# Kernel tuning notes

Measured on AMD Instinct MI355X. Metric: run time of the kernel, lower is better.

The kernel has to match this reference:

```python
import jax, jax.numpy as jnp
import numpy as np

B, S, V, D, H, C, NH = 8, 512, 32000, 768, 768, 9, 8
DH = D // NH


def setup_inputs() -> dict:
    key = jax.random.key(0)
    ks = list(jax.random.split(key, 24))
    it = iter(ks)

    def w(shape, s=0.02):
        return jax.random.normal(next(it), shape, jnp.float32) * s

    return {
        "input_ids": jax.random.randint(next(it), (B, S), 0, V, dtype=jnp.int32),
        "labels": jax.random.randint(next(it), (B, S), 0, C, dtype=jnp.int32),
        "emb_table": w((V, D), 1.0),
        "hw_Wh": w((D, D)),
        "hw_bh": jnp.zeros((D,), jnp.float32),
        "hw_Wt": w((D, D)),
        "hw_bt": jnp.zeros((D,), jnp.float32),
        "in_proj_w": w((3 * D, D)),
        "in_proj_b": jnp.zeros((3 * D,), jnp.float32),
        "out_proj_w": w((D, D)),
        "out_proj_b": jnp.zeros((D,), jnp.float32),
        "lstm0_Wih": w((2, 4 * H, D)),
        "lstm0_Whh": w((2, 4 * H, H)),
        "lstm0_b": jnp.zeros((2, 4 * H), jnp.float32),
        "lstm1_Wih": w((2, 4 * H, 2 * H)),
        "lstm1_Whh": w((2, 4 * H, H)),
        "lstm1_b": jnp.zeros((2, 4 * H), jnp.float32),
        "fc_W": w((C, 2 * H)),
        "fc_b": jnp.zeros((C,), jnp.float32),
        "crf_start": w((C,), 0.1),
        "crf_end": w((C,), 0.1),
        "crf_trans": w((C, C), 0.1),
    }


def _lstm_dir(x, Wih, Whh, b, reverse):
    # x: [B,S,in] -> outputs [B,S,H]; PyTorch gate order i,f,g,o
    xt = x.transpose(1, 0, 2)  # [S,B,in]
    h0 = jnp.zeros((x.shape[0], H), x.dtype)

    def step(carry, xt_):
        h, c = carry
        g = xt_ @ Wih.T + h @ Whh.T + b
        i, f, gg, o = jnp.split(g, 4, axis=-1)
        c = jax.nn.sigmoid(f) * c + jax.nn.sigmoid(i) * jnp.tanh(gg)
        h = jax.nn.sigmoid(o) * jnp.tanh(c)
        return (h, c), h

    _, hs = jax.lax.scan(step, (h0, h0), xt, reverse=reverse)
    return hs.transpose(1, 0, 2)


def _bilstm_layer(x, Wih, Whh, b):
    fwd = _lstm_dir(x, Wih[0], Whh[0], b[0], False)
    bwd = _lstm_dir(x, Wih[1], Whh[1], b[1], True)
    return jnp.concatenate([fwd, bwd], axis=-1)


def _emissions(input_ids, emb_table, hw_Wh, hw_bh, hw_Wt, hw_bt,
               in_proj_w, in_proj_b, out_proj_w, out_proj_b,
               lstm0_Wih, lstm0_Whh, lstm0_b, lstm1_Wih, lstm1_Whh, lstm1_b,
               fc_W, fc_b):
    x = emb_table[input_ids]  # [B,S,D]
    # Highway (1 layer, relu)
    hh = jax.nn.relu(x @ hw_Wh.T + hw_bh)
    t = jax.nn.sigmoid(x @ hw_Wt.T + hw_bt)
    x = t * hh + (1.0 - t) * x
    # Multi-head self-attention
    qkv = x @ in_proj_w.T + in_proj_b
    q, k, v = jnp.split(qkv, 3, axis=-1)
    hd = lambda a: a.reshape(B, S, NH, DH).transpose(0, 2, 1, 3)  # [B,NH,S,DH]
    q, k, v = hd(q), hd(k), hd(v)
    att = jax.nn.softmax(jnp.einsum('bhqd,bhkd->bhqk', q, k) / np.float32(np.sqrt(DH)), axis=-1)
    o = jnp.einsum('bhqk,bhkd->bhqd', att, v).transpose(0, 2, 1, 3).reshape(B, S, D)
    x = o @ out_proj_w.T + out_proj_b
    # 2-layer BiLSTM (inference: dropout off)
    x = _bilstm_layer(x, lstm0_Wih, lstm0_Whh, lstm0_b)
    x = _bilstm_layer(x, lstm1_Wih, lstm1_Whh, lstm1_b)
    return x @ fc_W.T + fc_b  # [B,S,C]


def _crf_nll(emissions, tags, crf_start, crf_end, crf_trans):
    # full mask (labels==-100 replaced by 0 before mask built), reduction='sum'
    em_t = emissions.transpose(1, 0, 2)  # [S,B,C]
    num = crf_start[tags[:, 0]] + crf_end[tags[:, -1]]
    num = num + jnp.take_along_axis(emissions, tags[..., None], axis=-1)[..., 0].sum(-1)
    num = num + crf_trans[tags[:, :-1], tags[:, 1:]].sum(-1)
    a0 = crf_start + em_t[0]  # [B,C]

    def fstep(a, em):
        a = jax.scipy.special.logsumexp(a[:, :, None] + crf_trans[None], axis=1) + em
        return a, None

    aT, _ = jax.lax.scan(fstep, a0, em_t[1:])
    logZ = jax.scipy.special.logsumexp(aT + crf_end, axis=-1)
    return -(num - logZ).sum()


def _viterbi(emissions, crf_start, crf_end, crf_trans):
    em_t = emissions.transpose(1, 0, 2)  # [S,B,C]
    s0 = crf_start + em_t[0]

    def vstep(s, em):
        sc = s[:, :, None] + crf_trans[None]  # [B,C_prev,C_next]
        return jnp.max(sc, axis=1) + em, jnp.argmax(sc, axis=1)

    sT, bps = jax.lax.scan(vstep, s0, em_t[1:])  # bps: [S-1,B,C]
    last = jnp.argmax(sT + crf_end, axis=-1)  # [B]

    def bstep(tag, bp):
        prev = jnp.take_along_axis(bp, tag[:, None], axis=1)[:, 0]
        return prev, prev

    _, path = jax.lax.scan(bstep, last, bps, reverse=True)  # [S-1,B]
    return jnp.concatenate([path, last[None]], axis=0).transpose(1, 0)  # [B,S]


def reference(input_ids, labels, emb_table, hw_Wh, hw_bh, hw_Wt, hw_bt,
              in_proj_w, in_proj_b, out_proj_w, out_proj_b,
              lstm0_Wih, lstm0_Whh, lstm0_b, lstm1_Wih, lstm1_Whh, lstm1_b,
              fc_W, fc_b, crf_start, crf_end, crf_trans):
    emissions = _emissions(input_ids, emb_table, hw_Wh, hw_bh, hw_Wt, hw_bt,
                           in_proj_w, in_proj_b, out_proj_w, out_proj_b,
                           lstm0_Wih, lstm0_Whh, lstm0_b,
                           lstm1_Wih, lstm1_Whh, lstm1_b, fc_W, fc_b)
    loss = _crf_nll(emissions, labels, crf_start, crf_end, crf_trans)
    decode = _viterbi(emissions, crf_start, crf_end, crf_trans)
    return loss, decode
```

## Files before the change

### kernel.cpp

```cpp
#include <hip/hip_runtime.h>
#include <hip/hip_bf16.h>
#include <cstdint>

#define B_   8
#define S_   512
#define D_   768
#define C_   9
#define BS_  4096

typedef unsigned long long u64;
typedef unsigned short ushort_t;
typedef short bf16x8 __attribute__((ext_vector_type(8)));
typedef float f32x4 __attribute__((ext_vector_type(4)));
typedef __attribute__((address_space(1))) const void gvoid_t;
typedef __attribute__((address_space(3))) void svoid_t;

__global__ __launch_bounds__(192) void k_embed(const int* __restrict__ ids,
                                               const float* __restrict__ emb,
                                               float* __restrict__ x) {
  int row = blockIdx.x;
  int id = ids[row];
  const float4* src = (const float4*)(emb + (size_t)id * D_);
  float4* dst = (float4*)(x + (size_t)row * D_);
  dst[threadIdx.x] = src[threadIdx.x];
}

#define GIDX(k, m) ((k)*144 + (m) + (((m) >> 5) << 2))

__global__ __launch_bounds__(256) void k_gemm(const float* __restrict__ A,
                                              const float* __restrict__ W,
                                              const float* __restrict__ bias,
                                              float* __restrict__ C,
                                              int M, int N, int K, int act, int mode) {
  __shared__ float As[2304];
  __shared__ float Bs[2304];
  int nwg = gridDim.x * gridDim.y;
  int lin = blockIdx.y * gridDim.x + blockIdx.x;
  int cpx = nwg >> 3;
  int swz = (lin & 7) * cpx + (lin >> 3);
  int bxs = swz % gridDim.x, bys = swz / gridDim.x;
  int bm0 = bys * 128, bn0 = bxs * 128;
  int tid = threadIdx.x;
  int tm = tid >> 4, tn = tid & 15;
  float acc[8][8];
#pragma unroll
  for (int i = 0; i < 8; ++i)
#pragma unroll
    for (int j = 0; j < 8; ++j) acc[i][j] = 0.f;

  for (int k0 = 0; k0 < K; k0 += 16) {
    __syncthreads();
#pragma unroll
    for (int j = 0; j < 2; ++j) {
      int f4 = tid + j * 256;
      int r = f4 >> 2;
      int kq = (f4 & 3) * 4;
      float4 va = *(const float4*)(A + (size_t)(bm0 + r) * K + k0 + kq);
      As[GIDX(kq + 0, r)] = va.x; As[GIDX(kq + 1, r)] = va.y;
      As[GIDX(kq + 2, r)] = va.z; As[GIDX(kq + 3, r)] = va.w;
      float4 vb = *(const float4*)(W + (size_t)(bn0 + r) * K + k0 + kq);
      Bs[GIDX(kq + 0, r)] = vb.x; Bs[GIDX(kq + 1, r)] = vb.y;
      Bs[GIDX(kq + 2, r)] = vb.z; Bs[GIDX(kq + 3, r)] = vb.w;
    }
    __syncthreads();
#pragma unroll
    for (int kk = 0; kk < 16; ++kk) {
      float a[8], b[8];
      *(float4*)&a[0] = *(const float4*)&As[GIDX(kk, tm * 8)];
      *(float4*)&a[4] = *(const float4*)&As[GIDX(kk, tm * 8 + 4)];
      *(float4*)&b[0] = *(const float4*)&Bs[GIDX(kk, tn * 8)];
      *(float4*)&b[4] = *(const float4*)&Bs[GIDX(kk, tn * 8 + 4)];
#pragma unroll
      for (int i = 0; i < 8; ++i)
#pragma unroll
        for (int j = 0; j < 8; ++j) acc[i][j] += a[i] * b[j];
    }
  }

  float bv[8];
#pragma unroll
  for (int j = 0; j < 8; ++j) bv[j] = bias[bn0 + tn * 8 + j];
#pragma unroll
  for (int i = 0; i < 8; ++i) {
    int row = bm0 + tm * 8 + i;
    float o[8];
#pragma unroll
    for (int j = 0; j < 8; ++j) {
      float v = acc[i][j] + bv[j];
      if (act == 1) v = fmaxf(v, 0.f);
      else if (act == 2) v = 1.f / (1.f + expf(-v));
      o[j] = v;
    }
    if (mode == 0) {
      float* cp = C + (size_t)row * N + bn0 + tn * 8;
      *(float4*)cp = make_float4(o[0], o[1], o[2], o[3]);
      *(float4*)(cp + 4) = make_float4(o[4], o[5], o[6], o[7]);
    } else {
      int bb = row >> 9, t = row & 511;
#pragma unroll
      for (int j = 0; j < 8; ++j) {
        unsigned n = bn0 + tn * 8 + j;
        unsigned dir = n / 3072u;
        unsigned n2 = n - dir * 3072u;
        unsigned g = n2 / 768u;
        unsigned rem = n2 - g * 768u;
        unsigned grp = rem >> 3, u = rem & 7;
        C[(((size_t)(dir * 512 + t) * 96 + grp) << 8) + u * 32 + g * 8 + bb] = o[j];
      }
    }
  }
}

__device__ inline ushort_t f2bf_bits(float x) {
  __hip_bfloat16 h = __float2bfloat16(x);
  return __builtin_bit_cast(ushort_t, h);
}
__device__ inline float bf2f(ushort_t b) {
  return __bfloat162float(__builtin_bit_cast(__hip_bfloat16, b));
}

__global__ __launch_bounds__(256) void k_cvt(const float* __restrict__ src,
                                             ushort_t* __restrict__ dst,
                                             int K, int total4, int mode) {
  int kq4 = K >> 2;
  for (int idx = blockIdx.x * 256 + threadIdx.x; idx < total4; idx += gridDim.x * 256) {
    int m = idx / kq4;
    int kq = (idx - m * kq4) * 4;
    float4 v = *(const float4*)(src + (size_t)m * K + kq);
    ushort4 hi, lo;
    hi.x = f2bf_bits(v.x); lo.x = f2bf_bits(v.x - bf2f(hi.x));
    hi.y = f2bf_bits(v.y); lo.y = f2bf_bits(v.y - bf2f(hi.y));
    hi.z = f2bf_bits(v.z); lo.z = f2bf_bits(v.z - bf2f(hi.z));
    hi.w = f2bf_bits(v.w); lo.w = f2bf_bits(v.w - bf2f(hi.w));
    ushort_t* base = dst + (size_t)m * 3 * K + kq;
    *(ushort4*)(base)         = hi;
    *(ushort4*)(base + K)     = mode ? hi : lo;
    *(ushort4*)(base + 2 * K) = mode ? lo : hi;
  }
}

__global__ __launch_bounds__(256) void k_mfma(const ushort_t* __restrict__ A,
                                              const ushort_t* __restrict__ W,
                                              const float* __restrict__ bias,
                                              float* __restrict__ C,
                                              int N, int Kp, int act, int mode) {
  __shared__ ushort_t Asb[128 * 64];
  __shared__ ushort_t Bsb[128 * 64];
  int nwg = gridDim.x * gridDim.y;
  int lin = blockIdx.y * gridDim.x + blockIdx.x;
  int cpx = nwg >> 3;
  int swz = (lin & 7) * cpx + (lin >> 3);
  int bn0 = (swz % gridDim.x) * 128, bm0 = (swz / gridDim.x) * 128;
  int tid = threadIdx.x;
  int w = tid >> 6, lane = tid & 63;
  int lr = lane & 15, lq = lane >> 4;

  f32x4 acc[2][8];
#pragma unroll
  for (int i = 0; i < 2; ++i)
#pragma unroll
    for (int j = 0; j < 8; ++j) acc[i][j] = (f32x4){0.f, 0.f, 0.f, 0.f};

  int srow0 = tid >> 3;
  int sc = tid & 7;

  for (int k0 = 0; k0 < Kp; k0 += 64) {
    __syncthreads();
#pragma unroll
    for (int it = 0; it < 4; ++it) {
      int row = it * 32 + srow0;
      int soff = (sc ^ (row & 7)) * 8;
      const ushort_t* ga = A + (size_t)(bm0 + row) * Kp + k0 + soff;
      const ushort_t* gb = W + (size_t)(bn0 + row) * Kp + k0 + soff;
      char* la = (char*)Asb + it * 4096 + (tid & 192) * 16;
      char* lb = (char*)Bsb + it * 4096 + (tid & 192) * 16;
      __builtin_amdgcn_global_load_lds((gvoid_t*)ga, (svoid_t*)la, 16, 0, 0);
      __builtin_amdgcn_global_load_lds((gvoid_t*)gb, (svoid_t*)lb, 16, 0, 0);
    }
    __syncthreads();
#pragma unroll
    for (int kf = 0; kf < 2; ++kf) {
      int c = kf * 4 + lq;
      int rowA0 = w * 32 + lr;
      int rowA1 = rowA0 + 16;
      bf16x8 a0 = *(const bf16x8*)&Asb[rowA0 * 64 + ((c ^ (rowA0 & 7)) << 3)];
      bf16x8 a1 = *(const bf16x8*)&Asb[rowA1 * 64 + ((c ^ (rowA1 & 7)) << 3)];
#pragma unroll
      for (int ns = 0; ns < 8; ++ns) {
        int rowB = ns * 16 + lr;
        bf16x8 b = *(const bf16x8*)&Bsb[rowB * 64 + ((c ^ (rowB & 7)) << 3)];
        acc[0][ns] = __builtin_amdgcn_mfma_f32_16x16x32_bf16(a0, b, acc[0][ns], 0, 0, 0);
        acc[1][ns] = __builtin_amdgcn_mfma_f32_16x16x32_bf16(a1, b, acc[1][ns], 0, 0, 0);
      }
    }
  }

  if (mode == 1) {
#pragma unroll
    for (int ns = 0; ns < 8; ++ns) {
      unsigned n = bn0 + ns * 16 + lr;
      unsigned dir = n / 3072u;
      unsigned n2 = n - dir * 3072u;
      unsigned g = n2 / 768u;
      unsigned rem = n2 - g * 768u;
      unsigned grp = rem >> 3, u = rem & 7;
      float bv = bias[n];
#pragma unroll
      for (int ms = 0; ms < 2; ++ms) {
#pragma unroll
        for (int r = 0; r < 4; ++r) {
          int m = bm0 + w * 32 + ms * 16 + lq * 4 + r;
          int bb = m >> 9, t = m & 511;
          C[(((size_t)(dir * 512 + t) * 96 + grp) << 8) + u * 32 + g * 8 + bb] =
              acc[ms][ns][r] + bv;
        }
      }
    }
  } else {
#pragma unroll
    for (int ns = 0; ns < 8; ++ns) {
      int col = bn0 + ns * 16 + lr;
      float bv = bias[col];
#pragma unroll
      for (int ms = 0; ms < 2; ++ms) {
#pragma unroll
        for (int r = 0; r < 4; ++r) {
          int m = bm0 + w * 32 + ms * 16 + lq * 4 + r;
          float v = acc[ms][ns][r] + bv;
          if (act == 1) v = fmaxf(v, 0.f);
          else if (act == 2) v = 1.f / (1.f + expf(-v));
          C[(size_t)m * N + col] = v;
        }
      }
    }
  }
}

__global__ __launch_bounds__(256) void k_highway(float* __restrict__ x,
                                                 const float* __restrict__ hh,
                                                 const float* __restrict__ tt) {
  const int n4 = BS_ * D_ / 4;
  for (int i = blockIdx.x * 256 + threadIdx.x; i < n4; i += gridDim.x * 256) {
    float4 xv = ((const float4*)x)[i];
    float4 hv = ((const float4*)hh)[i];
    float4 tv = ((const float4*)tt)[i];
    xv.x = tv.x * hv.x + (1.f - tv.x) * xv.x;
    xv.y = tv.y * hv.y + (1.f - tv.y) * xv.y;
    xv.z = tv.z * hv.z + (1.f - tv.z) * xv.z;
    xv.w = tv.w * hv.w + (1.f - tv.w) * xv.w;
    ((float4*)x)[i] = xv;
  }
}

__global__ __launch_bounds__(256) void k_attn(const float* __restrict__ qkv,
                                              float* __restrict__ out) {
  __shared__ float Qs[16 * 100];
  __shared__ float Ks[32 * 101];
  __shared__ float Ps[16 * 513];
  int bh = blockIdx.x;
  int b = bh >> 3, h = bh & 7;
  int q0 = blockIdx.y * 16;
  int tid = threadIdx.x;
  const float scale = 0.10206207261596577f;

  const float* qb = qkv + (size_t)(b * 512 + q0) * 2304 + h * 96;
  for (int i = tid; i < 16 * 96; i += 256) {
    int r = i / 96, c = i - r * 96;
    Qs[r * 100 + c] = qb[(size_t)r * 2304 + c];
  }
  int qi = tid >> 4, kseg = tid & 15;

  for (int kt = 0; kt < 16; ++kt) {
    __syncthreads();
    const float* kb = qkv + (size_t)(b * 512 + kt * 32) * 2304 + 768 + h * 96;
    for (int i = tid; i < 32 * 96; i += 256) {
      int r = i / 96, c = i - r * 96;
      Ks[r * 101 + c] = kb[(size_t)r * 2304 + c];
    }
    __syncthreads();
    int kj0 = kseg * 2;
    float s0 = 0.f, s1 = 0.f;
    const float* qrow = &Qs[qi * 100];
    const float* k0p = &Ks[kj0 * 101];
    const float* k1p = &Ks[(kj0 + 1) * 101];
#pragma unroll 8
    for (int d = 0; d < 96; ++d) {
      float qv = qrow[d];
      s0 += qv * k0p[d];
      s1 += qv * k1p[d];
    }
    Ps[qi * 513 + kt * 32 + kj0] = s0 * scale;
    Ps[qi * 513 + kt * 32 + kj0 + 1] = s1 * scale;
  }
  __syncthreads();

  {
    float m = -1e30f;
    for (int j = 0; j < 32; ++j) m = fmaxf(m, Ps[qi * 513 + kseg + j * 16]);
    m = fmaxf(m, __shfl_xor(m, 1)); m = fmaxf(m, __shfl_xor(m, 2));
    m = fmaxf(m, __shfl_xor(m, 4)); m = fmaxf(m, __shfl_xor(m, 8));
    float sum = 0.f;
    for (int j = 0; j < 32; ++j) {
      int idx = qi * 513 + kseg + j * 16;
      float e = expf(Ps[idx] - m);
      Ps[idx] = e;
      sum += e;
    }
    sum += __shfl_xor(sum, 1); sum += __shfl_xor(sum, 2);
    sum += __shfl_xor(sum, 4); sum += __shfl_xor(sum, 8);
    float inv = 1.f / sum;
    for (int j = 0; j < 32; ++j) Ps[qi * 513 + kseg + j * 16] *= inv;
  }

  float acc[6] = {0.f, 0.f, 0.f, 0.f, 0.f, 0.f};
  int d0 = kseg * 6;
  for (int kt = 0; kt < 16; ++kt) {
    __syncthreads();
    const float* vb = qkv + (size_t)(b * 512 + kt * 32) * 2304 + 1536 + h * 96;
    for (int i = tid; i < 32 * 96; i += 256) {
      int r = i / 96, c = i - r * 96;
      Ks[r * 101 + c] = vb[(size_t)r * 2304 + c];
    }
    __syncthreads();
#pragma unroll 4
    for (int kj = 0; kj < 32; ++kj) {
      float p = Ps[qi * 513 + kt * 32 + kj];
      const float* vrow = &Ks[kj * 101 + d0];
#pragma unroll
      for (int u = 0; u < 6; ++u) acc[u] += p * vrow[u];
    }
  }
  float* ob = out + (size_t)(b * 512 + q0 + qi) * 768 + h * 96 + d0;
#pragma unroll
  for (int u = 0; u < 6; ++u) ob[u] = acc[u];
}

#define NWGD 96
__global__ __launch_bounds__(256, 1) void k_lstm(const float* __restrict__ gates,
                                                 const float* __restrict__ Whh,
                                                 float* __restrict__ hbuf,
                                                 float* __restrict__ hs,
                                                 int* __restrict__ flags) {
  __shared__ float hlds[8 * 772];
  int tid = threadIdx.x;
  int wg = blockIdx.x;
  int dir = wg / NWGD;
  int grp = wg % NWGD;
  int rg = tid >> 5;
  int ks = tid & 31;

  float4 w4[4][6];
#pragma unroll
  for (int j = 0; j < 4; ++j) {
    const float* wp = Whh + ((size_t)dir * 3072 + j * 768 + grp * 8 + rg) * 768 + ks * 4;
#pragma unroll
    for (int jj = 0; jj < 6; ++jj)
      w4[j][jj] = *(const float4*)(wp + jj * 128);
  }

  float* hb = hbuf + (size_t)dir * 2 * 6144;
  const float* gbase = gates + (size_t)dir * 512 * 24576 + grp * 256 + tid;
  const float* hp = hlds + ks * 4;
  float cst = 0.f;

  for (int step = 0; step < 512; ++step) {
    int t = dir ? (511 - step) : step;
    float gqv = gbase[(size_t)t * 24576];

#pragma unroll
    for (int i = 0; i < 3; ++i) {
      int idx = i * 256 + tid;
      int b2 = idx / 96;
      int kq = (idx - b2 * 96) * 8;
      const u64* src = (const u64*)(hb + (step & 1) * 6144 + b2 * 768 + kq);
      u64 lo  = __hip_atomic_load(src + 0, __ATOMIC_RELAXED, __HIP_MEMORY_SCOPE_AGENT);
      u64 hi  = __hip_atomic_load(src + 1, __ATOMIC_RELAXED, __HIP_MEMORY_SCOPE_AGENT);
      u64 lo2 = __hip_atomic_load(src + 2, __ATOMIC_RELAXED, __HIP_MEMORY_SCOPE_AGENT);
      u64 hi2 = __hip_atomic_load(src + 3, __ATOMIC_RELAXED, __HIP_MEMORY_SCOPE_AGENT);
      float* dst = &hlds[b2 * 772 + kq];
      *(u64*)(dst + 0) = lo;
      *(u64*)(dst + 2) = hi;
      *(u64*)(dst + 4) = lo2;
      *(u64*)(dst + 6) = hi2;
    }
    __syncthreads();

    float v[32];
#pragma unroll
    for (int i = 0; i < 32; ++i) v[i] = 0.f;
#pragma unroll
    for (int jj = 0; jj < 6; ++jj) {
#pragma unroll
      for (int b2 = 0; b2 < 8; ++b2) {
        float4 hv = *(const float4*)(hp + b2 * 772 + jj * 128);
#pragma unroll
        for (int j = 0; j < 4; ++j) {
          float4 w = w4[j][jj];
          v[j * 8 + b2] = fmaf(w.x, hv.x, v[j * 8 + b2]);
          v[j * 8 + b2] = fmaf(w.y, hv.y, v[j * 8 + b2]);
          v[j * 8 + b2] = fmaf(w.z, hv.z, v[j * 8 + b2]);
          v[j * 8 + b2] = fmaf(w.w, hv.w, v[j * 8 + b2]);
        }
      }
    }

    {
      bool hi = (ks & 16) != 0;
#pragma unroll
      for (int i = 0; i < 16; ++i) {
        float keep = hi ? v[i + 16] : v[i];
        float send = hi ? v[i] : v[i + 16];
        v[i] = keep + __shfl_xor(send, 16);
      }
    }
    {
      bool hi = (ks & 8) != 0;
#pragma unroll
      for (int i = 0; i < 8; ++i) {
        float keep = hi ? v[i + 8] : v[i];
        float send = hi ? v[i] : v[i + 8];
        v[i] = keep + __shfl_xor(send, 8);
      }
    }
    {
      bool hi = (ks & 4) != 0;
#pragma unroll
      for (int i = 0; i < 4; ++i) {
        float keep = hi ? v[i + 4] : v[i];
        float send = hi ? v[i] : v[i + 4];
        v[i] = keep + __shfl_xor(send, 4);
      }
    }
    {
      bool hi = (ks & 2) != 0;
#pragma unroll
      for (int i = 0; i < 2; ++i) {
        float keep = hi ? v[i + 2] : v[i];
        float send = hi ? v[i] : v[i + 2];
        v[i] = keep + __shfl_xor(send, 2);
      }
    }
    {
      bool hi = (ks & 1) != 0;
      float keep = hi ? v[1] : v[0];
      float send = hi ? v[0] : v[1];
      v[0] = keep + __shfl_xor(send, 1);
    }

    float gv = v[0] + gqv;
    float gf = __shfl_down(gv, 8);
    float gg = __shfl_down(gv, 16);
    float go = __shfl_down(gv, 24);
    float hnew = 0.f;
    if (ks < 8) {
      float i_ = 1.f / (1.f + expf(-gv));
      float f_ = 1.f / (1.f + expf(-gf));
      float ci = tanhf(gg);
      float o_ = 1.f / (1.f + expf(-go));
      cst = f_ * cst + i_ * ci;
      hnew = o_ * tanhf(cst);
      __hip_atomic_store(hb + (size_t)((step + 1) & 1) * 6144 + ks * 768 + grp * 8 + rg,
                         hnew, __ATOMIC_RELAXED, __HIP_MEMORY_SCOPE_AGENT);
    }

    __syncthreads();
    if (tid == 0)
      __hip_atomic_store(&flags[wg * 32], step + 1, __ATOMIC_RELAXED, __HIP_MEMORY_SCOPE_AGENT);
    if (ks < 8)
      hs[((size_t)(ks * 512 + t)) * 1536 + dir * 768 + grp * 8 + rg] = hnew;
    if (tid < NWGD) {
      const int* fp = &flags[(dir * NWGD + tid) * 32];
      while (__hip_atomic_load(fp, __ATOMIC_RELAXED, __HIP_MEMORY_SCOPE_AGENT) <= step)
        __builtin_amdgcn_s_sleep(2);
    }
    __syncthreads();
  }
}

__global__ __launch_bounds__(256) void k_fc(const float* __restrict__ A,
                                            const float* __restrict__ Wf,
                                            const float* __restrict__ bf,
                                            float* __restrict__ out) {
  __shared__ float Wl[9 * 1536];
  int tid = threadIdx.x;
  for (int i = tid; i < 9 * 1536; i += 256) Wl[i] = Wf[i];
  __syncthreads();
  int lane = tid & 63, wv = tid >> 6;
  int row = blockIdx.x * 4 + wv;
  const float* a = A + (size_t)row * 1536;
  float acc[9];
#pragma unroll
  for (int c = 0; c < 9; ++c) acc[c] = 0.f;
  for (int i = 0; i < 24; ++i) {
    float av = a[lane + i * 64];
#pragma unroll
    for (int c = 0; c < 9; ++c) acc[c] += av * Wl[c * 1536 + lane + i * 64];
  }
#pragma unroll
  for (int c = 0; c < 9; ++c) {
#pragma unroll
    for (int m = 1; m < 64; m <<= 1) acc[c] += __shfl_xor(acc[c], m);
  }
  if (lane == 0) {
#pragma unroll
    for (int c = 0; c < 9; ++c) out[(size_t)row * 9 + c] = acc[c] + bf[c];
  }
}

__global__ __launch_bounds__(512) void k_crf(const float* __restrict__ em,
                                             const int* __restrict__ labels,
                                             const float* __restrict__ cs,
                                             const float* __restrict__ ce,
                                             const float* __restrict__ ct,
                                             float* __restrict__ out) {
  __shared__ float trans_s[81];
  __shared__ unsigned char bps[8][511][12];
  __shared__ float partres[16];
  int tid = threadIdx.x;
  int b = tid >> 6;
  int lane = tid & 63;
  bool act = lane < 9;
  if (tid < 81) trans_s[tid] = ct[tid];
  __syncthreads();

  float tcol[9];
#pragma unroll
  for (int cp = 0; cp < 9; ++cp) tcol[cp] = act ? trans_s[cp * 9 + lane] : 0.f;

  float a_ = -1e30f, v_ = -1e30f;
  if (act) {
    float e0 = em[((size_t)b * 512) * 9 + lane];
    a_ = cs[lane] + e0;
    v_ = a_;
  }

  float e = act ? em[((size_t)b * 512 + 1) * 9 + lane] : 0.f;
  for (int t = 1; t < 512; ++t) {
    float e_nxt = 0.f;
    if (act && t < 511) e_nxt = em[((size_t)b * 512 + t + 1) * 9 + lane];
    float m = -1e30f, vm = -1e30f;
    int bp = 0;
    float xs[9];
#pragma unroll
    for (int cp = 0; cp < 9; ++cp) {
      float ap = __shfl(a_, cp);
      float vp = __shfl(v_, cp);
      float x = ap + tcol[cp];
      xs[cp] = x;
      m = fmaxf(m, x);
      float y = vp + tcol[cp];
      if (y > vm) { vm = y; bp = cp; }
    }
    float ssum = 0.f;
#pragma unroll
    for (int cp = 0; cp < 9; ++cp) ssum += expf(xs[cp] - m);
    if (act) {
      a_ = m + logf(ssum) + e;
      v_ = vm + e;
      bps[b][t - 1][lane] = (unsigned char)bp;
    }
    e = e_nxt;
  }

  float fin = act ? a_ + ce[lane] : -1e30f;
  float vfin = act ? v_ + ce[lane] : -1e30f;
  float m2 = fin;
  m2 = fmaxf(m2, __shfl_xor(m2, 1)); m2 = fmaxf(m2, __shfl_xor(m2, 2));
  m2 = fmaxf(m2, __shfl_xor(m2, 4)); m2 = fmaxf(m2, __shfl_xor(m2, 8));
  float s2 = expf(fin - m2);
  s2 += __shfl_xor(s2, 1); s2 += __shfl_xor(s2, 2);
  s2 += __shfl_xor(s2, 4); s2 += __shfl_xor(s2, 8);
  float logZ = m2 + logf(s2);

  float bv = vfin; int bi = lane;
#pragma unroll
  for (int s = 1; s < 16; s <<= 1) {
    float ov = __shfl_xor(bv, s);
    int oi = __shfl_xor(bi, s);
    if (ov > bv || (ov == bv && oi < bi)) { bv = ov; bi = oi; }
  }

  float np = 0.f;
  for (int t = lane; t < 512; t += 64) {
    int tg = labels[b * 512 + t];
    np += em[((size_t)b * 512 + t) * 9 + tg];
    if (t < 511) np += trans_s[tg * 9 + labels[b * 512 + t + 1]];
  }
#pragma unroll
  for (int s = 1; s < 64; s <<= 1) np += __shfl_xor(np, s);

  if (lane == 0) {
    np += cs[labels[b * 512]] + ce[labels[b * 512 + 511]];
    partres[b] = np;
    partres[8 + b] = logZ;
    out[1 + b * 512 + 511] = (float)bi;
    int tg = bi;
    for (int t = 510; t >= 0; --t) {
      tg = bps[b][t][tg];
      out[1 + b * 512 + t] = (float)tg;
    }
  }
  __syncthreads();
  if (tid == 0) {
    float acc = 0.f;
#pragma unroll
    for (int b2 = 0; b2 < 8; ++b2) acc += partres[b2] - partres[8 + b2];
    out[0] = -acc;
  }
}

extern "C" void kernel_launch(void* const* d_in, const int* in_sizes, int n_in,
                              void* d_out, int out_size, void* d_ws, size_t ws_size,
                              hipStream_t stream) {
  (void)in_sizes; (void)n_in; (void)out_size;
  const int*   ids    = (const int*)d_in[0];
  const int*   labels = (const int*)d_in[1];
  const float* emb    = (const float*)d_in[2];
  const float* hwWh   = (const float*)d_in[3];
  const float* hwbh   = (const float*)d_in[4];
  const float* hwWt   = (const float*)d_in[5];
  const float* hwbt   = (const float*)d_in[6];
  const float* ipw    = (const float*)d_in[7];
  const float* ipb    = (const float*)d_in[8];
  const float* opw    = (const float*)d_in[9];
  const float* opb    = (const float*)d_in[10];
  const float* l0Wih  = (const float*)d_in[11];
  const float* l0Whh  = (const float*)d_in[12];
  const float* l0b    = (const float*)d_in[13];
  const float* l1Wih  = (const float*)d_in[14];
  const float* l1Whh  = (const float*)d_in[15];
  const float* l1b    = (const float*)d_in[16];
  const float* fcW    = (const float*)d_in[17];
  const float* fcb    = (const float*)d_in[18];
  const float* cs     = (const float*)d_in[19];
  const float* ce     = (const float*)d_in[20];
  const float* ct     = (const float*)d_in[21];

  float* ws   = (float*)d_ws;
  float* x0   = ws;
  float* gbuf = ws + 3145728;
  float* hh   = gbuf;
  float* tt   = gbuf + 3145728;
  float* qkv  = gbuf + 6291456;
  float* x1   = ws + 28311552;
  float* hs0  = ws + 31457280;
  float* hs1  = ws + 37748736;
  float* em   = ws + 44040192;
  float* hbuf = ws + 44077056;
  int*   flags = (int*)(ws + 44101632);
  ushort_t* bfA = (ushort_t*)(ws + 44107776);
  ushort_t* bfW = (ushort_t*)(ws + 44107776 + 9437184);
  const size_t ws_need = (44107776ull + 9437184ull + 14155776ull) * 4ull;
  bool bf16path = (ws_size >= ws_need);

  dim3 g768(6, 32), g2304(18, 32), g6144(48, 32);

  k_embed<<<BS_, 192, 0, stream>>>(ids, emb, x0);

  if (bf16path) {
    k_cvt<<<2048, 256, 0, stream>>>(x0, bfA, 768, BS_ * 768 / 4, 0);
    k_cvt<<<2048, 256, 0, stream>>>(hwWh, bfW, 768, 768 * 768 / 4, 1);
    k_mfma<<<g768, 256, 0, stream>>>(bfA, bfW, hwbh, hh, 768, 2304, 1, 0);
    k_cvt<<<2048, 256, 0, stream>>>(hwWt, bfW, 768, 768 * 768 / 4, 1);
    k_mfma<<<g768, 256, 0, stream>>>(bfA, bfW, hwbt, tt, 768, 2304, 2, 0);
    k_highway<<<768, 256, 0, stream>>>(x0, hh, tt);
    k_cvt<<<2048, 256, 0, stream>>>(x0, bfA, 768, BS_ * 768 / 4, 0);
    k_cvt<<<2048, 256, 0, stream>>>(ipw, bfW, 768, 2304 * 768 / 4, 1);
    k_mfma<<<g2304, 256, 0, stream>>>(bfA, bfW, ipb, qkv, 2304, 2304, 0, 0);
    k_attn<<<dim3(64, 32), 256, 0, stream>>>(qkv, x0);
    k_cvt<<<2048, 256, 0, stream>>>(x0, bfA, 768, BS_ * 768 / 4, 0);
    k_cvt<<<2048, 256, 0, stream>>>(opw, bfW, 768, 768 * 768 / 4, 1);
    k_mfma<<<g768, 256, 0, stream>>>(bfA, bfW, opb, x1, 768, 2304, 0, 0);
    k_cvt<<<2048, 256, 0, stream>>>(x1, bfA, 768, BS_ * 768 / 4, 0);
    k_cvt<<<2048, 256, 0, stream>>>(l0Wih, bfW, 768, 6144 * 768 / 4, 1);
    k_mfma<<<g6144, 256, 0, stream>>>(bfA, bfW, l0b, gbuf, 6144, 2304, 0, 1);
  } else {
    k_gemm<<<g768, 256, 0, stream>>>(x0, hwWh, hwbh, hh, BS_, 768, 768, 1, 0);
    k_gemm<<<g768, 256, 0, stream>>>(x0, hwWt, hwbt, tt, BS_, 768, 768, 2, 0);
    k_highway<<<768, 256, 0, stream>>>(x0, hh, tt);
    k_gemm<<<g2304, 256, 0, stream>>>(x0, ipw, ipb, qkv, BS_, 2304, 768, 0, 0);
    k_attn<<<dim3(64, 32), 256, 0, stream>>>(qkv, x0);
    k_gemm<<<g768, 256, 0, stream>>>(x0, opw, opb, x1, BS_, 768, 768, 0, 0);
    k_gemm<<<g6144, 256, 0, stream>>>(x1, l0Wih, l0b, gbuf, BS_, 6144, 768, 0, 1);
  }
  hipMemsetAsync(hbuf, 0, (24576 + 192 * 32) * sizeof(float), stream);
  k_lstm<<<192, 256, 0, stream>>>(gbuf, l0Whh, hbuf, hs0, flags);

  if (bf16path) {
    k_cvt<<<2048, 256, 0, stream>>>(hs0, bfA, 1536, BS_ * 1536 / 4, 0);
    k_cvt<<<4096, 256, 0, stream>>>(l1Wih, bfW, 1536, 6144 * 1536 / 4, 1);
    k_mfma<<<g6144, 256, 0, stream>>>(bfA, bfW, l1b, gbuf, 6144, 4608, 0, 1);
  } else {
    k_gemm<<<g6144, 256, 0, stream>>>(hs0, l1Wih, l1b, gbuf, BS_, 6144, 1536, 0, 1);
  }
  hipMemsetAsync(hbuf, 0, (24576 + 192 * 32) * sizeof(float), stream);
  k_lstm<<<192, 256, 0, stream>>>(gbuf, l1Whh, hbuf, hs1, flags);

  k_fc<<<1024, 256, 0, stream>>>(hs1, fcW, fcb, em);
  k_crf<<<1, 512, 0, stream>>>(em, labels, cs, ce, ct, (float*)d_out);
}
```

Baseline: 7.186 ms.

## Fuse layer-0 input projection into persistent LSTM kernel and emit bf16 hidden states

Adds a persistent layer-0 LSTM kernel that keeps its slice of the input-projection weights in LDS and computes x_t·Wih for the next step between recurrence steps, overlapping it with the cross-workgroup barrier wait. This removes the separate layer-0 input GEMM, its conversion kernels and the gate buffer round-trip. The kernel also writes the hidden states directly as split bf16 hi/lo pairs in the layout the layer-1 MFMA GEMM expects, so the hs0 conversion pass is no longer needed. The cost is extra per-step FMA work and LDS traffic on the serial critical path, plus large register pressure from holding the recurrent weights and partial sums.

```diff
diff --git a/kernel.cpp b/kernel.cpp
--- a/kernel.cpp
+++ b/kernel.cpp
@@ -468,6 +468,248 @@
       __hip_atomic_store(&flags[wg * 32], step + 1, __ATOMIC_RELAXED, __HIP_MEMORY_SCOPE_AGENT);
     if (ks < 8)
       hs[((size_t)(ks * 512 + t)) * 1536 + dir * 768 + grp * 8 + rg] = hnew;
+    if (tid < NWGD) {
+      const int* fp = &flags[(dir * NWGD + tid) * 32];
+      while (__hip_atomic_load(fp, __ATOMIC_RELAXED, __HIP_MEMORY_SCOPE_AGENT) <= step)
+        __builtin_amdgcn_s_sleep(2);
+    }
+    __syncthreads();
+  }
+}
+
+__global__ __launch_bounds__(256, 1) void k_lstm_f0(const float* __restrict__ x,
+                                                    const float* __restrict__ Wih,
+                                                    const float* __restrict__ bih,
+                                                    const float* __restrict__ Whh,
+                                                    float* __restrict__ hbuf,
+                                                    ushort_t* __restrict__ hs_bf,
+                                                    int* __restrict__ flags) {
+  __shared__ float hlds[8 * 772];
+  __shared__ float xlds[8 * 772];
+  __shared__ float wlds[32 * 772];
+  int tid = threadIdx.x;
+  int wg = blockIdx.x;
+  int dir = wg / NWGD;
+  int grp = wg % NWGD;
+  int rg = tid >> 5;
+  int ks = tid & 31;
+
+  float4 w4[4][6];
+#pragma unroll
+  for (int j = 0; j < 4; ++j) {
+    const float* wp = Whh + ((size_t)dir * 3072 + j * 768 + grp * 8 + rg) * 768 + ks * 4;
+#pragma unroll
+    for (int jj = 0; jj < 6; ++jj)
+      w4[j][jj] = *(const float4*)(wp + jj * 128);
+  }
+  for (int it = 0; it < 24; ++it) {
+    int f4i = it * 256 + tid;
+    int rowL = f4i / 192;
+    int kq = (f4i - rowL * 192) * 4;
+    int j = rowL >> 3, rgl = rowL & 7;
+    float4 v = *(const float4*)(Wih + ((size_t)dir * 3072 + j * 768 + grp * 8 + rgl) * 768 + kq);
+    *(float4*)&wlds[rowL * 772 + kq] = v;
+  }
+  float bi = bih[dir * 3072 + (ks >> 3) * 768 + grp * 8 + rg];
+
+  float* hb = hbuf + (size_t)dir * 2 * 6144;
+  const float* hp = hlds + ks * 4;
+  float cst = 0.f;
+
+  int t0 = dir ? 511 : 0;
+  for (int i = 0; i < 6; ++i) {
+    int idx = i * 256 + tid;
+    int b2 = idx / 192;
+    int kq = (idx - b2 * 192) * 4;
+    *(float4*)&xlds[b2 * 772 + kq] =
+        *(const float4*)(x + ((size_t)(b2 * 512 + t0)) * 768 + kq);
+  }
+  __syncthreads();
+
+  float vx[32];
+#pragma unroll
+  for (int i = 0; i < 32; ++i) vx[i] = 0.f;
+#pragma unroll
+  for (int jj = 0; jj < 6; ++jj) {
+    float4 wv[4];
+#pragma unroll
+    for (int j = 0; j < 4; ++j)
+      wv[j] = *(const float4*)&wlds[(j * 8 + rg) * 772 + jj * 128 + ks * 4];
+#pragma unroll
+    for (int b2 = 0; b2 < 8; ++b2) {
+      float4 xv = *(const float4*)&xlds[b2 * 772 + jj * 128 + ks * 4];
+#pragma unroll
+      for (int j = 0; j < 4; ++j) {
+        vx[j * 8 + b2] = fmaf(wv[j].x, xv.x, vx[j * 8 + b2]);
+        vx[j * 8 + b2] = fmaf(wv[j].y, xv.y, vx[j * 8 + b2]);
+        vx[j * 8 + b2] = fmaf(wv[j].z, xv.z, vx[j * 8 + b2]);
+        vx[j * 8 + b2] = fmaf(wv[j].w, xv.w, vx[j * 8 + b2]);
+      }
+    }
+  }
+  float4 xreg[6];
+  {
+    int t1 = dir ? 510 : 1;
+    for (int i = 0; i < 6; ++i) {
+      int idx = i * 256 + tid;
+      int b2 = idx / 192;
+      int kq = (idx - b2 * 192) * 4;
+      xreg[i] = *(const float4*)(x + ((size_t)(b2 * 512 + t1)) * 768 + kq);
+    }
+  }
+
+  for (int step = 0; step < 512; ++step) {
+    int t = dir ? (511 - step) : step;
+
+#pragma unroll
+    for (int i = 0; i < 3; ++i) {
+      int idx = i * 256 + tid;
+      int b2 = idx / 96;
+      int kq = (idx - b2 * 96) * 8;
+      const u64* src = (const u64*)(hb + (step & 1) * 6144 + b2 * 768 + kq);
+      u64 lo  = __hip_atomic_load(src + 0, __ATOMIC_RELAXED, __HIP_MEMORY_SCOPE_AGENT);
+      u64 hi  = __hip_atomic_load(src + 1, __ATOMIC_RELAXED, __HIP_MEMORY_SCOPE_AGENT);
+      u64 lo2 = __hip_atomic_load(src + 2, __ATOMIC_RELAXED, __HIP_MEMORY_SCOPE_AGENT);
+      u64 hi2 = __hip_atomic_load(src + 3, __ATOMIC_RELAXED, __HIP_MEMORY_SCOPE_AGENT);
+      float* dst = &hlds[b2 * 772 + kq];
+      *(u64*)(dst + 0) = lo;
+      *(u64*)(dst + 2) = hi;
+      *(u64*)(dst + 4) = lo2;
+      *(u64*)(dst + 6) = hi2;
+    }
+    __syncthreads();
+
+    if (step < 511) {
+#pragma unroll
+      for (int i = 0; i < 6; ++i) {
+        int idx = i * 256 + tid;
+        int b2 = idx / 192;
+        int kq = (idx - b2 * 192) * 4;
+        *(float4*)&xlds[b2 * 772 + kq] = xreg[i];
+      }
+    }
+
+    float v[32];
+#pragma unroll
+    for (int i = 0; i < 32; ++i) v[i] = vx[i];
+#pragma unroll
+    for (int jj = 0; jj < 6; ++jj) {
+#pragma unroll
+      for (int b2 = 0; b2 < 8; ++b2) {
+        float4 hv = *(const float4*)(hp + b2 * 772 + jj * 128);
+#pragma unroll
+        for (int j = 0; j < 4; ++j) {
+          float4 w = w4[j][jj];
+          v[j * 8 + b2] = fmaf(w.x, hv.x, v[j * 8 + b2]);
+          v[j * 8 + b2] = fmaf(w.y, hv.y, v[j * 8 + b2]);
+          v[j * 8 + b2] = fmaf(w.z, hv.z, v[j * 8 + b2]);
+          v[j * 8 + b2] = fmaf(w.w, hv.w, v[j * 8 + b2]);
+        }
+      }
+    }
+
+    {
+      bool hi = (ks & 16) != 0;
+#pragma unroll
+      for (int i = 0; i < 16; ++i) {
+        float keep = hi ? v[i + 16] : v[i];
+        float send = hi ? v[i] : v[i + 16];
+        v[i] = keep + __shfl_xor(send, 16);
+      }
+    }
+    {
+      bool hi = (ks & 8) != 0;
+#pragma unroll
+      for (int i = 0; i < 8; ++i) {
+        float keep = hi ? v[i + 8] : v[i];
+        float send = hi ? v[i] : v[i + 8];
+        v[i] = keep + __shfl_xor(send, 8);
+      }
+    }
+    {
+      bool hi = (ks & 4) != 0;
+#pragma unroll
+      for (int i = 0; i < 4; ++i) {
+        float keep = hi ? v[i + 4] : v[i];
+        float send = hi ? v[i] : v[i + 4];
+        v[i] = keep + __shfl_xor(send, 4);
+      }
+    }
+    {
+      bool hi = (ks & 2) != 0;
+#pragma unroll
+      for (int i = 0; i < 2; ++i) {
+        float keep = hi ? v[i + 2] : v[i];
+        float send = hi ? v[i] : v[i + 2];
+        v[i] = keep + __shfl_xor(send, 2);
+      }
+    }
+    {
+      bool hi = (ks & 1) != 0;
+      float keep = hi ? v[1] : v[0];
+      float send = hi ? v[0] : v[1];
+      v[0] = keep + __shfl_xor(send, 1);
+    }
+
+    float gv = v[0] + bi;
+    float gf = __shfl_down(gv, 8);
+    float gg = __shfl_down(gv, 16);
+    float go = __shfl_down(gv, 24);
+    float hnew = 0.f;
+    if (ks < 8) {
+      float i_ = 1.f / (1.f + expf(-gv));
+      float f_ = 1.f / (1.f + expf(-gf));
+      float ci = tanhf(gg);
+      float o_ = 1.f / (1.f + expf(-go));
+      cst = f_ * cst + i_ * ci;
+      hnew = o_ * tanhf(cst);
+      __hip_atomic_store(hb + (size_t)((step + 1) & 1) * 6144 + ks * 768 + grp * 8 + rg,
+                         hnew, __ATOMIC_RELAXED, __HIP_MEMORY_SCOPE_AGENT);
+    }
+
+    __syncthreads();
+    if (tid == 0)
+      __hip_atomic_store(&flags[wg * 32], step + 1, __ATOMIC_RELAXED, __HIP_MEMORY_SCOPE_AGENT);
+    if (ks < 8) {
+      ushort_t hi16 = f2bf_bits(hnew);
+      ushort_t lo16 = f2bf_bits(hnew - bf2f(hi16));
+      size_t base = ((size_t)(ks * 512 + t)) * 4608 + dir * 768 + grp * 8 + rg;
+      hs_bf[base] = hi16;
+      hs_bf[base + 1536] = lo16;
+      hs_bf[base + 3072] = hi16;
+    }
+    if (step < 511) {
+#pragma unroll
+      for (int i = 0; i < 32; ++i) vx[i] = 0.f;
+#pragma unroll
+      for (int jj = 0; jj < 6; ++jj) {
+        float4 wv[4];
+#pragma unroll
+        for (int j = 0; j < 4; ++j)
+          wv[j] = *(const float4*)&wlds[(j * 8 + rg) * 772 + jj * 128 + ks * 4];
+#pragma unroll
+        for (int b2 = 0; b2 < 8; ++b2) {
+          float4 xv = *(const float4*)&xlds[b2 * 772 + jj * 128 + ks * 4];
+#pragma unroll
+          for (int j = 0; j < 4; ++j) {
+            vx[j * 8 + b2] = fmaf(wv[j].x, xv.x, vx[j * 8 + b2]);
+            vx[j * 8 + b2] = fmaf(wv[j].y, xv.y, vx[j * 8 + b2]);
+            vx[j * 8 + b2] = fmaf(wv[j].z, xv.z, vx[j * 8 + b2]);
+            vx[j * 8 + b2] = fmaf(wv[j].w, xv.w, vx[j * 8 + b2]);
+          }
+        }
+      }
+    }
+    if (step < 510) {
+      int tn = dir ? (509 - step) : (step + 2);
+#pragma unroll
+      for (int i = 0; i < 6; ++i) {
+        int idx = i * 256 + tid;
+        int b2 = idx / 192;
+        int kq = (idx - b2 * 192) * 4;
+        xreg[i] = *(const float4*)(x + ((size_t)(b2 * 512 + tn)) * 768 + kq);
+      }
+    }
     if (tid < NWGD) {
       const int* fp = &flags[(dir * NWGD + tid) * 32];
       while (__hip_atomic_load(fp, __ATOMIC_RELAXED, __HIP_MEMORY_SCOPE_AGENT) <= step)
@@ -671,9 +913,14 @@
     k_cvt<<<2048, 256, 0, stream>>>(x0, bfA, 768, BS_ * 768 / 4, 0);
     k_cvt<<<2048, 256, 0, stream>>>(opw, bfW, 768, 768 * 768 / 4, 1);
     k_mfma<<<g768, 256, 0, stream>>>(bfA, bfW, opb, x1, 768, 2304, 0, 0);
-    k_cvt<<<2048, 256, 0, stream>>>(x1, bfA, 768, BS_ * 768 / 4, 0);
-    k_cvt<<<2048, 256, 0, stream>>>(l0Wih, bfW, 768, 6144 * 768 / 4, 1);
-    k_mfma<<<g6144, 256, 0, stream>>>(bfA, bfW, l0b, gbuf, 6144, 2304, 0, 1);
+
+    hipMemsetAsync(hbuf, 0, (24576 + 192 * 32) * sizeof(float), stream);
+    k_lstm_f0<<<192, 256, 0, stream>>>(x1, l0Wih, l0b, l0Whh, hbuf, bfA, flags);
+
+    k_cvt<<<4096, 256, 0, stream>>>(l1Wih, bfW, 1536, 6144 * 1536 / 4, 1);
+    k_mfma<<<g6144, 256, 0, stream>>>(bfA, bfW, l1b, gbuf, 6144, 4608, 0, 1);
+    hipMemsetAsync(hbuf, 0, (24576 + 192 * 32) * sizeof(float), stream);
+    k_lstm<<<192, 256, 0, stream>>>(gbuf, l1Whh, hbuf, hs1, flags);
   } else {
     k_gemm<<<g768, 256, 0, stream>>>(x0, hwWh, hwbh, hh, BS_, 768, 768, 1, 0);
     k_gemm<<<g768, 256, 0, stream>>>(x0, hwWt, hwbt, tt, BS_, 768, 768, 2, 0);
@@ -682,19 +929,12 @@
     k_attn<<<dim3(64, 32), 256, 0, stream>>>(qkv, x0);
     k_gemm<<<g768, 256, 0, stream>>>(x0, opw, opb, x1, BS_, 768, 768, 0, 0);
     k_gemm<<<g6144, 256, 0, stream>>>(x1, l0Wih, l0b, gbuf, BS_, 6144, 768, 0, 1);
-  }
-  hipMemsetAsync(hbuf, 0, (24576 + 192 * 32) * sizeof(float), stream);
-  k_lstm<<<192, 256, 0, stream>>>(gbuf, l0Whh, hbuf, hs0, flags);
-
-  if (bf16path) {
-    k_cvt<<<2048, 256, 0, stream>>>(hs0, bfA, 1536, BS_ * 1536 / 4, 0);
-    k_cvt<<<4096, 256, 0, stream>>>(l1Wih, bfW, 1536, 6144 * 1536 / 4, 1);
-    k_mfma<<<g6144, 256, 0, stream>>>(bfA, bfW, l1b, gbuf, 6144, 4608, 0, 1);
-  } else {
+    hipMemsetAsync(hbuf, 0, (24576 + 192 * 32) * sizeof(float), stream);
+    k_lstm<<<192, 256, 0, stream>>>(gbuf, l0Whh, hbuf, hs0, flags);
     k_gemm<<<g6144, 256, 0, stream>>>(hs0, l1Wih, l1b, gbuf, BS_, 6144, 1536, 0, 1);
-  }
-  hipMemsetAsync(hbuf, 0, (24576 + 192 * 32) * sizeof(float), stream);
-  k_lstm<<<192, 256, 0, stream>>>(gbuf, l1Whh, hbuf, hs1, flags);
+    hipMemsetAsync(hbuf, 0, (24576 + 192 * 32) * sizeof(float), stream);
+    k_lstm<<<192, 256, 0, stream>>>(gbuf, l1Whh, hbuf, hs1, flags);
+  }
 
   k_fc<<<1024, 256, 0, stream>>>(hs1, fcW, fcb, em);
   k_crf<<<1, 512, 0, stream>>>(em, labels, cs, ce, ct, (float*)d_out);
```

New measurement: 7.810 ms. 1.09x slower.
